# Kernel tuning notes

Measured on AMD Instinct MI355X. Metric: run time of the kernel, lower is better.

Reference implementation:

```python
import jax, jax.numpy as jnp
import numpy as np

TEMP = 0.1


def _e8_roots() -> np.ndarray:
    # Type 1: (+-1, +-1, 0^6) in all coordinate pairs -> 112 roots
    r1 = []
    for i in range(8):
        for j in range(i + 1, 8):
            for si in (-1.0, 1.0):
                for sj in (-1.0, 1.0):
                    v = np.zeros(8, dtype=np.float32)
                    v[i] = si
                    v[j] = sj
                    r1.append(v)
    # Type 2: all +-0.5 with an even number of minus signs -> 128 roots
    r2 = []
    for mask in range(256):
        bits = [(mask >> b) & 1 for b in range(8)]
        if sum(bits) % 2 == 0:
            r2.append([-0.5 if b else 0.5 for b in bits])
    roots = np.concatenate([np.stack(r1), np.asarray(r2, dtype=np.float32)], axis=0)
    assert roots.shape == (240, 8)
    # Module applies F.normalize(p=2, dim=1) to the raw roots -> unit norm rows
    roots = roots / np.linalg.norm(roots, axis=1, keepdims=True)
    return roots.astype(np.float32)


def setup_inputs() -> dict:
    key = jax.random.key(0)
    x = jax.random.normal(key, (256, 4096, 8), dtype=jnp.float32)
    roots = jnp.asarray(_e8_roots())  # [240, 8], unit-norm
    return {"x": x, "roots": roots}


def reference(x, roots):
    x_norm_sq = jnp.sum(x * x, axis=-1, keepdims=True)      # [..., 1]
    roots_norm_sq = jnp.sum(roots * roots, axis=-1)          # [240]
    cross = jnp.einsum("btd,kd->btk", x, roots)             # [B, T, 240]
    distances = x_norm_sq - 2.0 * cross + roots_norm_sq      # [B, T, 240]
    weights = jax.nn.softmax(-distances / TEMP, axis=-1)     # [B, T, 240]
    quantized = jnp.einsum("btk,kd->btd", weights, roots)    # [B, T, 8]
    # Straight-through: value = quantized, gradient = identity w.r.t. x
    return x + jax.lax.stop_gradient(quantized - x)
```

## Files before the change

### kernel.cpp

```cpp
#include <hip/hip_runtime.h>
#include <math.h>

#define BLOCK 256

typedef float v4f __attribute__((ext_vector_type(4)));

struct EO { float E, O; };
__device__ __forceinline__ EO mergeEO(EO a, EO b) {
    EO r;
    r.E = fmaf(a.E, b.E, a.O * b.O);
    r.O = fmaf(a.E, b.O, a.O * b.E);
    return r;
}

__global__ __launch_bounds__(BLOCK) void e8q_kernel(const float* __restrict__ x,
                                                    float* __restrict__ out) {
    const size_t t = (size_t)blockIdx.x * BLOCK + threadIdx.x;

    const v4f* xp = (const v4f*)(x + t * 8);
    v4f xv0 = xp[0];
    v4f xv1 = xp[1];
    float xs[8] = {xv0.x, xv0.y, xv0.z, xv0.w, xv1.x, xv1.y, xv1.z, xv1.w};

    float n2 = 0.0f;
#pragma unroll
    for (int j = 0; j < 8; ++j) n2 = fmaf(xs[j], xs[j], n2);
    const float xn = __builtin_amdgcn_sqrtf(n2);

    const float K2 = 10.201358186637847f;
    const float C  = 28.853900817779268f * xn;
    const float Ce = 0.125f * C;
    const float s  = __builtin_amdgcn_exp2f(-0.25f * C);

    float A[8], B[8], g[8], h[8];
#pragma unroll
    for (int j = 0; j < 8; ++j) {
        g[j] = __builtin_amdgcn_exp2f(fmaf(K2, xs[j], -Ce));
        h[j] = __builtin_amdgcn_exp2f(fmaf(-K2, xs[j], -Ce));
        float a = g[j] * g[j];
        float b = h[j] * h[j];
        float sa = s * a;
        A[j] = fmaf(s, b, sa);
        B[j] = fmaf(-s, b, sa);
    }

    float preA[8], sufA[8];
    preA[0] = A[0];
#pragma unroll
    for (int j = 1; j < 8; ++j) preA[j] = preA[j - 1] + A[j];
    sufA[7] = A[7];
#pragma unroll
    for (int j = 6; j >= 0; --j) sufA[j] = sufA[j + 1] + A[j];

    float EA[8];
    EA[0] = sufA[1];
    EA[7] = preA[6];
#pragma unroll
    for (int j = 1; j < 7; ++j) EA[j] = preA[j - 1] + sufA[j + 1];

    float s1 = 0.0f;
#pragma unroll
    for (int j = 0; j < 7; ++j) s1 = fmaf(A[j], sufA[j + 1], s1);

    EO pre[8], suf[8];
    pre[0] = {g[0], h[0]};
#pragma unroll
    for (int j = 1; j < 8; ++j) pre[j] = mergeEO(pre[j - 1], {g[j], h[j]});
    suf[7] = {g[7], h[7]};
#pragma unroll
    for (int j = 6; j >= 1; --j) suf[j] = mergeEO({g[j], h[j]}, suf[j + 1]);

    const float s2 = pre[7].E;

    EO ex[8];
    ex[0] = suf[1];
    ex[7] = pre[6];
#pragma unroll
    for (int j = 1; j < 7; ++j) ex[j] = mergeEO(pre[j - 1], suf[j + 1]);

    const float inv = __builtin_amdgcn_rcpf(s1 + s2);
    const float c1 = 0.70710678118654752f * inv;
    const float c2 = 0.35355339059327376f * inv;

    float o[8];
#pragma unroll
    for (int j = 0; j < 8; ++j) {
        float t1 = B[j] * EA[j];
        float t2 = fmaf(g[j], ex[j].E, -(h[j] * ex[j].O));
        o[j] = fmaf(c1, t1, c2 * t2);
    }

    v4f o0 = {o[0], o[1], o[2], o[3]};
    v4f o1 = {o[4], o[5], o[6], o[7]};
    v4f* op = (v4f*)(out + t * 8);
    __builtin_nontemporal_store(o0, op);
    __builtin_nontemporal_store(o1, op + 1);
}

extern "C" void kernel_launch(void* const* d_in, const int* in_sizes, int n_in,
                              void* d_out, int out_size, void* d_ws, size_t ws_size,
                              hipStream_t stream) {
    const float* x = (const float*)d_in[0];
    float* out = (float*)d_out;

    const int tokens = in_sizes[0] / 8;
    const int grid = tokens / BLOCK;

    e8q_kernel<<<grid, BLOCK, 0, stream>>>(x, out);
}
```

Baseline: 16.23 us.

## Stage outputs through LDS for coalesced stores and compute prefixes on the fly

Each thread now writes its 8 outputs into shared memory, and after a barrier the block writes them back so consecutive threads store consecutive 16-byte chunks. This is meant to give fully coalesced nontemporal stores. The prefix arrays are computed incrementally inside the output loop instead of stored, which lowers register pressure, and launch bounds now ask for 6 blocks per CU. The cost is an LDS round trip and a block-wide barrier on a kernel that is otherwise purely streaming.

```diff
diff --git a/kernel.cpp b/kernel.cpp
--- a/kernel.cpp
+++ b/kernel.cpp
@@ -13,15 +13,7 @@
     return r;
 }
 
-__global__ __launch_bounds__(BLOCK) void e8q_kernel(const float* __restrict__ x,
-                                                    float* __restrict__ out) {
-    const size_t t = (size_t)blockIdx.x * BLOCK + threadIdx.x;
-
-    const v4f* xp = (const v4f*)(x + t * 8);
-    v4f xv0 = xp[0];
-    v4f xv1 = xp[1];
-    float xs[8] = {xv0.x, xv0.y, xv0.z, xv0.w, xv1.x, xv1.y, xv1.z, xv1.w};
-
+__device__ __forceinline__ void e8q_token(const float xs[8], float o[8]) {
     float n2 = 0.0f;
 #pragma unroll
     for (int j = 0; j < 8; ++j) n2 = fmaf(xs[j], xs[j], n2);
@@ -44,57 +36,83 @@
         B[j] = fmaf(-s, b, sa);
     }
 
-    float preA[8], sufA[8];
-    preA[0] = A[0];
-#pragma unroll
-    for (int j = 1; j < 8; ++j) preA[j] = preA[j - 1] + A[j];
+    float sufA[8];
     sufA[7] = A[7];
 #pragma unroll
     for (int j = 6; j >= 0; --j) sufA[j] = sufA[j + 1] + A[j];
-
-    float EA[8];
-    EA[0] = sufA[1];
-    EA[7] = preA[6];
-#pragma unroll
-    for (int j = 1; j < 7; ++j) EA[j] = preA[j - 1] + sufA[j + 1];
 
     float s1 = 0.0f;
 #pragma unroll
     for (int j = 0; j < 7; ++j) s1 = fmaf(A[j], sufA[j + 1], s1);
 
-    EO pre[8], suf[8];
-    pre[0] = {g[0], h[0]};
-#pragma unroll
-    for (int j = 1; j < 8; ++j) pre[j] = mergeEO(pre[j - 1], {g[j], h[j]});
+    EO suf[8];
     suf[7] = {g[7], h[7]};
 #pragma unroll
     for (int j = 6; j >= 1; --j) suf[j] = mergeEO({g[j], h[j]}, suf[j + 1]);
 
-    const float s2 = pre[7].E;
-
-    EO ex[8];
-    ex[0] = suf[1];
-    ex[7] = pre[6];
-#pragma unroll
-    for (int j = 1; j < 7; ++j) ex[j] = mergeEO(pre[j - 1], suf[j + 1]);
+    const float s2 = mergeEO({g[0], h[0]}, suf[1]).E;
 
     const float inv = __builtin_amdgcn_rcpf(s1 + s2);
     const float c1 = 0.70710678118654752f * inv;
     const float c2 = 0.35355339059327376f * inv;
 
-    float o[8];
+    float preA = 0.0f;
+    EO preEO;
 #pragma unroll
     for (int j = 0; j < 8; ++j) {
-        float t1 = B[j] * EA[j];
-        float t2 = fmaf(g[j], ex[j].E, -(h[j] * ex[j].O));
-        o[j] = fmaf(c1, t1, c2 * t2);
+        float EA;
+        EO ex;
+        if (j == 0) {
+            EA = sufA[1];
+            ex = suf[1];
+        } else if (j == 7) {
+            EA = preA;
+            ex = preEO;
+        } else {
+            EA = preA + sufA[j + 1];
+            ex = mergeEO(preEO, suf[j + 1]);
+        }
+        float t2 = fmaf(g[j], ex.E, -(h[j] * ex.O));
+        o[j] = fmaf(c1 * B[j], EA, c2 * t2);
+
+        if (j == 0) {
+            preA = A[0];
+            preEO = {g[0], h[0]};
+        } else {
+            preA += A[j];
+            preEO = mergeEO(preEO, {g[j], h[j]});
+        }
     }
+}
 
-    v4f o0 = {o[0], o[1], o[2], o[3]};
-    v4f o1 = {o[4], o[5], o[6], o[7]};
-    v4f* op = (v4f*)(out + t * 8);
-    __builtin_nontemporal_store(o0, op);
-    __builtin_nontemporal_store(o1, op + 1);
+__global__ __launch_bounds__(BLOCK, 6) void e8q_kernel(const float* __restrict__ x,
+                                                       float* __restrict__ out) {
+    __shared__ v4f lA[BLOCK];
+    __shared__ v4f lB[BLOCK];
+
+    const int tid = threadIdx.x;
+    const size_t tok0 = (size_t)blockIdx.x * BLOCK;
+
+    const v4f* xp = (const v4f*)(x + (tok0 + tid) * 8);
+    v4f a = xp[0];
+    v4f b = xp[1];
+    float xs[8] = {a.x, a.y, a.z, a.w, b.x, b.y, b.z, b.w};
+
+    float o[8];
+    e8q_token(xs, o);
+
+    lA[tid] = (v4f){o[0], o[1], o[2], o[3]};
+    lB[tid] = (v4f){o[4], o[5], o[6], o[7]};
+
+    __syncthreads();
+
+    v4f* outp = (v4f*)out + tok0 * 2;
+#pragma unroll
+    for (int k = 0; k < 2; ++k) {
+        const int sidx = k * BLOCK + tid;
+        v4f val = ((sidx & 1) ? lB : lA)[sidx >> 1];
+        __builtin_nontemporal_store(val, outp + sidx);
+    }
 }
 
 extern "C" void kernel_launch(void* const* d_in, const int* in_sizes, int n_in,
```

Result: faster. 14.92 us (-8.1%).
